# Kernel optimization log

Hardware: AMD Instinct MI355X
Metric: run time of the kernel (lower is better)

The kernel has to match this reference:

```python
import jax, jax.numpy as jnp
import numpy as np

B, D_MODEL, N, H = 4, 256, 2048, 4
HEAD_DIM = D_MODEL // H  # 64


def _rotate_half(x):
    # x: [..., d] with d even; pairs (x1, x2) -> (-x2, x1)
    x = x.reshape(x.shape[:-1] + (x.shape[-1] // 2, 2))
    x1, x2 = x[..., 0], x[..., 1]
    return jnp.stack((-x2, x1), axis=-1).reshape(x.shape[:-2] + (-1,))


def _apply_rope(freqs, t):
    # freqs: [2, n, d] (cos, sin); t: [b, h, n, d]
    return t * freqs[0] + _rotate_half(t) * freqs[1]


def setup_inputs() -> dict:
    key = jax.random.key(0)
    ks = jax.random.split(key, 12)
    s = 0.02
    inp = {
        "query": jax.random.normal(ks[0], (B, D_MODEL, N), jnp.float32),
        "key": jax.random.normal(ks[1], (B, D_MODEL, N), jnp.float32),
        "value": jax.random.normal(ks[2], (B, D_MODEL, N), jnp.float32),
        "encoding": jax.random.normal(ks[3], (2, N, HEAD_DIM), jnp.float32),
        "Wq": jax.random.normal(ks[4], (D_MODEL, D_MODEL), jnp.float32) * s,
        "bq": jnp.zeros((D_MODEL,), jnp.float32),
        "Wk": jax.random.normal(ks[5], (D_MODEL, D_MODEL), jnp.float32) * s,
        "bk": jnp.zeros((D_MODEL,), jnp.float32),
        "Wv": jax.random.normal(ks[6], (D_MODEL, D_MODEL), jnp.float32) * s,
        "bv": jnp.zeros((D_MODEL,), jnp.float32),
        "Wm": jax.random.normal(ks[7], (D_MODEL, D_MODEL), jnp.float32) * s,
        "bm": jnp.zeros((D_MODEL,), jnp.float32),
    }
    return inp


def _proj(W, b, x):
    # 1x1 Conv1d == channel matmul: x [b, c_in, n] -> [b, c_out, n]
    return jnp.einsum('oi,bin->bon', W, x) + b[None, :, None]


def reference(query, key, value, encoding, Wq, bq, Wk, bk, Wv, bv, Wm, bm):
    b = query.shape[0]
    # project and split channels into (head_dim, heads): [b, d, h, n]
    q = _proj(Wq, bq, query).reshape(b, HEAD_DIM, H, -1)
    k = _proj(Wk, bk, key).reshape(b, HEAD_DIM, H, -1)
    v = _proj(Wv, bv, value).reshape(b, HEAD_DIM, H, -1)
    # RoPE on [b, h, n, d] layout
    q = jnp.transpose(_apply_rope(encoding, jnp.transpose(q, (0, 2, 3, 1))), (0, 3, 1, 2))
    k = jnp.transpose(_apply_rope(encoding, jnp.transpose(k, (0, 2, 3, 1))), (0, 3, 1, 2))
    # attention: scores [b, h, n, m]
    scores = jnp.einsum('bdhn,bdhm->bhnm', q, k) / jnp.sqrt(jnp.float32(HEAD_DIM))
    prob = jax.nn.softmax(scores, axis=-1)
    x = jnp.einsum('bhnm,bdhm->bdhn', prob, v)
    x = x.reshape(b, HEAD_DIM * H, -1)
    return _proj(Wm, bm, x)
```

## Files before the change

kernel.cpp:

```cpp
#include <hip/hip_runtime.h>
#include <stdint.h>

#define NSEQ 2048

typedef __attribute__((ext_vector_type(4))) float f32x4;
typedef __attribute__((ext_vector_type(8))) short s16x8;
typedef _Float16 f16x8 __attribute__((ext_vector_type(8)));

#define OFF_XT  0u
#define OFF_XA  0u
#define OFF_PO  4194304u
#define OFF_W   12582912u
#define OFF_QR  13107200u
#define OFF_KR  17301504u
#define OFF_VT  21495808u
#define OFF_M   25690112u
#define OFF_L   25952256u

__device__ __forceinline__ short f2h(float f) {
  _Float16 h = (_Float16)f;
  return __builtin_bit_cast(short, h);
}
__device__ __forceinline__ float h2f(short s) {
  return (float)__builtin_bit_cast(_Float16, s);
}
__device__ __forceinline__ int swz64(int row, int slot) {
  return row * 64 + ((slot ^ ((row >> 1) & 3)) << 4);
}
__device__ __forceinline__ int swz128(int row, int slot) {
  return row * 128 + ((slot ^ (row & 7)) << 4);
}
#define MFMA(a, b, c) __builtin_amdgcn_mfma_f32_16x16x32_f16(a, b, c, 0, 0, 0)

__global__ void k_convw(const float* __restrict__ Wq, const float* __restrict__ Wk,
                        const float* __restrict__ Wv, const float* __restrict__ Wm,
                        char* __restrict__ ws) {
  int o = blockIdx.x, which = blockIdx.y, i = threadIdx.x;
  const float* src = which == 0 ? Wq : which == 1 ? Wk : which == 2 ? Wv : Wm;
  short* dst = (short*)(ws + OFF_W) + which * 65536;
  float val = (which < 3) ? src[o * 256 + i] : src[o * 256 + ((i & 63) << 2) + (i >> 6)];
  dst[o * 256 + i] = f2h(val);
}

__global__ __launch_bounds__(256) void k_trans(const float* __restrict__ q,
    const float* __restrict__ k, const float* __restrict__ v, char* __restrict__ ws) {
  int tensor = blockIdx.z >> 2, b = blockIdx.z & 3;
  const float* src = tensor == 0 ? q : (tensor == 1 ? k : v);
  short* dst = (short*)(ws + OFF_XT) + (tensor * 4 + b) * 524288;
  int n0 = blockIdx.x * 64, i0 = blockIdx.y * 64;
  __shared__ float tile[64][65];
  int t = threadIdx.x;
  int nl = t & 63, ib = (t >> 6) * 16;
#pragma unroll
  for (int r = 0; r < 16; ++r)
    tile[ib + r][nl] = src[(b * 256 + i0 + ib + r) * 2048 + n0 + nl];
  __syncthreads();
  int nr = t >> 2, ic = (t & 3) * 16;
  short tmp[16];
#pragma unroll
  for (int j = 0; j < 16; ++j) tmp[j] = f2h(tile[ic + j][nr]);
  short* dp = &dst[(n0 + nr) * 256 + i0 + ic];
  *(s16x8*)dp = *(const s16x8*)&tmp[0];
  *(s16x8*)(dp + 8) = *(const s16x8*)&tmp[8];
}

__device__ __forceinline__ void gemm128(const short* __restrict__ W, const short* __restrict__ X,
                                        int o0, int n0, short* As, short* Bs, f32x4 acc[4][4]) {
  int t = threadIdx.x;
  int lane = t & 63, g = lane >> 4, c = lane & 15, wave = t >> 6;
  int wo = (wave >> 1) * 64, wn = (wave & 1) * 64;
  int row = t >> 2, slot = t & 3;
  for (int kk = 0; kk < 8; ++kk) {
    __syncthreads();
    int koff = kk * 32 + slot * 8;
    *(s16x8*)((char*)As + swz64(row, slot))      = *(const s16x8*)&W[(o0 + row) * 256 + koff];
    *(s16x8*)((char*)As + swz64(row + 64, slot)) = *(const s16x8*)&W[(o0 + row + 64) * 256 + koff];
    *(s16x8*)((char*)Bs + swz64(row, slot))      = *(const s16x8*)&X[(n0 + row) * 256 + koff];
    *(s16x8*)((char*)Bs + swz64(row + 64, slot)) = *(const s16x8*)&X[(n0 + row + 64) * 256 + koff];
    __syncthreads();
    f16x8 af[4], bfr[4];
#pragma unroll
    for (int f = 0; f < 4; ++f) {
      af[f]  = *(const f16x8*)((char*)As + swz64(wo + f * 16 + c, g));
      bfr[f] = *(const f16x8*)((char*)Bs + swz64(wn + f * 16 + c, g));
    }
#pragma unroll
    for (int i = 0; i < 4; ++i)
#pragma unroll
      for (int j = 0; j < 4; ++j)
        acc[i][j] = MFMA(af[i], bfr[j], acc[i][j]);
  }
}

__global__ __launch_bounds__(256) void k_proj(const float* __restrict__ enc,
    const float* __restrict__ bq, const float* __restrict__ bk, const float* __restrict__ bv,
    char* __restrict__ ws) {
  int proj = blockIdx.z >> 2, b = blockIdx.z & 3;
  const short* W = (const short*)(ws + OFF_W) + proj * 65536;
  const short* X = (const short*)(ws + OFF_XT) + (proj * 4 + b) * 524288;
  int o0 = blockIdx.y * 128, n0 = blockIdx.x * 128;
  __shared__ short As[128 * 32], Bs[128 * 32];
  f32x4 acc[4][4] = {};
  gemm128(W, X, o0, n0, As, Bs, acc);
  int t = threadIdx.x, lane = t & 63, g = lane >> 4, c = lane & 15, wave = t >> 6;
  int wo = (wave >> 1) * 64, wn = (wave & 1) * 64;
  const float* bias = proj == 0 ? bq : (proj == 1 ? bk : bv);
  if (proj < 2) {
    short* dst = (short*)(ws + (proj == 0 ? OFF_QR : OFF_KR));
    float scale = proj == 0 ? 0.125f : 1.0f;
    float sgn = (g & 1) ? 1.0f : -1.0f;
#pragma unroll
    for (int i = 0; i < 4; ++i) {
      int ob = o0 + wo + i * 16 + g * 4;
      int d = ob >> 2;
#pragma unroll
      for (int j = 0; j < 4; ++j) {
        int n = n0 + wn + j * 16 + c;
        float cv = enc[n * 64 + d], sv = enc[131072 + n * 64 + d];
#pragma unroll
        for (int r = 0; r < 4; ++r) {
          float val = acc[i][j][r] + bias[ob + r];
          float par = __shfl_xor(val, 16, 64);
          float res = (val * cv + sgn * par * sv) * scale;
          dst[((b * 4 + r) * 2048 + n) * 64 + d] = f2h(res);
        }
      }
    }
  } else {
    short* dst = (short*)(ws + OFF_VT);
#pragma unroll
    for (int i = 0; i < 4; ++i) {
      int ob = o0 + wo + i * 16 + g * 4;
      int d = ob >> 2;
#pragma unroll
      for (int j = 0; j < 4; ++j) {
        int n = n0 + wn + j * 16 + c;
#pragma unroll
        for (int r = 0; r < 4; ++r) {
          float val = acc[i][j][r] + bias[ob + r];
          dst[((b * 4 + r) * 64 + d) * 2048 + n] = f2h(val);
        }
      }
    }
  }
}

__global__ __launch_bounds__(256, 4) void k_attn(char* __restrict__ ws) {
  int bh = blockIdx.y, ms = blockIdx.z;
  int t = threadIdx.x, wave = t >> 6, lane = t & 63, g = lane >> 4, c = lane & 15;
  int nw = blockIdx.x * 64 + wave * 16;
  const short* Q = (const short*)(ws + OFF_QR) + bh * 131072;
  const short* K = (const short*)(ws + OFF_KR) + bh * 131072;
  const short* V = (const short*)(ws + OFF_VT) + bh * 131072;
  __shared__ short Ks[64 * 64], Vs[64 * 64], Ps[4][16 * 64];
  char* Pb = (char*)Ps[wave];
  f16x8 qf0 = *(const f16x8*)&Q[(nw + c) * 64 + g * 8];
  f16x8 qf1 = *(const f16x8*)&Q[(nw + c) * 64 + 32 + g * 8];
  f32x4 po[4] = {};
  float mrun[4], lrun[4];
#pragma unroll
  for (int r = 0; r < 4; ++r) { mrun[r] = -1e30f; lrun[r] = 0.f; }
  int sr = t >> 3, sl = t & 7;
  const int mb = ms * 1024;

  s16x8 rk0, rk1, rv0, rv1, sk0, sk1, sv0, sv1;
  auto LD = [&](int m0, s16x8& a, s16x8& b2, s16x8& c2, s16x8& d2) {
    a  = *(const s16x8*)&K[(m0 + sr) * 64 + sl * 8];
    b2 = *(const s16x8*)&K[(m0 + sr + 32) * 64 + sl * 8];
    c2 = *(const s16x8*)&V[sr * 2048 + m0 + sl * 8];
    d2 = *(const s16x8*)&V[(sr + 32) * 2048 + m0 + sl * 8];
  };
  auto ST = [&](const s16x8& a, const s16x8& b2, const s16x8& c2, const s16x8& d2) {
    *(s16x8*)((char*)Ks + swz128(sr, sl))      = a;
    *(s16x8*)((char*)Ks + swz128(sr + 32, sl)) = b2;
    *(s16x8*)((char*)Vs + swz128(sr, sl))      = c2;
    *(s16x8*)((char*)Vs + swz128(sr + 32, sl)) = d2;
  };
  auto COMPUTE = [&]() {
    f32x4 s[4] = {};
    __builtin_amdgcn_s_setprio(1);
#pragma unroll
    for (int fj = 0; fj < 4; ++fj) {
      f16x8 k0 = *(const f16x8*)((char*)Ks + swz128(fj * 16 + c, g));
      f16x8 k1 = *(const f16x8*)((char*)Ks + swz128(fj * 16 + c, 4 + g));
      s[fj] = MFMA(qf0, k0, s[fj]);
      s[fj] = MFMA(qf1, k1, s[fj]);
    }
    __builtin_amdgcn_s_setprio(0);
    float pm[4], nm[4], corr[4], rs[4];
#pragma unroll
    for (int r = 0; r < 4; ++r) {
      pm[r] = fmaxf(fmaxf(s[0][r], s[1][r]), fmaxf(s[2][r], s[3][r]));
#pragma unroll
      for (int d_ = 1; d_ < 16; d_ <<= 1) pm[r] = fmaxf(pm[r], __shfl_xor(pm[r], d_, 64));
      nm[r] = fmaxf(mrun[r], pm[r]);
      corr[r] = __expf(mrun[r] - nm[r]);
      mrun[r] = nm[r];
      rs[r] = 0.f;
    }
    float p[4][4];
#pragma unroll
    for (int fj = 0; fj < 4; ++fj)
#pragma unroll
      for (int r = 0; r < 4; ++r) {
        p[fj][r] = __expf(s[fj][r] - nm[r]);
        rs[r] += p[fj][r];
      }
#pragma unroll
    for (int r = 0; r < 4; ++r) {
#pragma unroll
      for (int d_ = 1; d_ < 16; d_ <<= 1) rs[r] += __shfl_xor(rs[r], d_, 64);
      lrun[r] = lrun[r] * corr[r] + rs[r];
    }
#pragma unroll
    for (int fd = 0; fd < 4; ++fd)
#pragma unroll
      for (int r = 0; r < 4; ++r) po[fd][r] *= corr[r];
#pragma unroll
    for (int fj = 0; fj < 4; ++fj)
#pragma unroll
      for (int r = 0; r < 4; ++r) {
        int rr = g * 4 + r, mm = fj * 16 + c;
        *(short*)(Pb + swz128(rr, mm >> 3) + (mm & 7) * 2) = f2h(p[fj][r]);
      }
    asm volatile("s_waitcnt lgkmcnt(0)" ::: "memory");
    __builtin_amdgcn_sched_barrier(0);
    f16x8 pa0 = *(const f16x8*)(Pb + swz128(c, g));
    f16x8 pa1 = *(const f16x8*)(Pb + swz128(c, 4 + g));
    __builtin_amdgcn_s_setprio(1);
#pragma unroll
    for (int fd = 0; fd < 4; ++fd) {
      int dd = fd * 16 + c;
      f16x8 vb0 = *(const f16x8*)((char*)Vs + swz128(dd, g));
      f16x8 vb1 = *(const f16x8*)((char*)Vs + swz128(dd, 4 + g));
      po[fd] = MFMA(pa0, vb0, po[fd]);
      po[fd] = MFMA(pa1, vb1, po[fd]);
    }
    __builtin_amdgcn_s_setprio(0);
  };

  LD(mb, rk0, rk1, rv0, rv1);
  for (int tt = 0; tt < 16; tt += 2) {
    __syncthreads();
    ST(rk0, rk1, rv0, rv1);
    LD(mb + (tt + 1) * 64, sk0, sk1, sv0, sv1);
    __syncthreads();
    COMPUTE();
    __syncthreads();
    ST(sk0, sk1, sv0, sv1);
    if (tt + 2 < 16) LD(mb + (tt + 2) * 64, rk0, rk1, rv0, rv1);
    __syncthreads();
    COMPUTE();
  }

  short* PO = (short*)(ws + OFF_PO);
  float* Mm = (float*)(ws + OFF_M);
  float* Ll = (float*)(ws + OFF_L);
  int base = (ms * 16 + bh) * 2048;
#pragma unroll
  for (int fd = 0; fd < 4; ++fd) {
    int d = fd * 16 + c;
#pragma unroll
    for (int r = 0; r < 4; ++r) {
      int n = nw + g * 4 + r;
      PO[(base + n) * 64 + d] = f2h(po[fd][r] / lrun[r]);
    }
  }
  if (c == 0) {
#pragma unroll
    for (int r = 0; r < 4; ++r) {
      int n = nw + g * 4 + r;
      Mm[base + n] = mrun[r];
      Ll[base + n] = lrun[r];
    }
  }
}

__global__ __launch_bounds__(256) void k_comb(char* __restrict__ ws) {
  int t = threadIdx.x;
  int row = blockIdx.x * 32 + (t >> 3);
  int bh = row >> 11, n = row & 2047;
  int dc = (t & 7) * 8;
  const short* PO = (const short*)(ws + OFF_PO);
  const float* Mm = (const float*)(ws + OFF_M);
  const float* Ll = (const float*)(ws + OFF_L);
  float m1 = Mm[row], m2 = Mm[32768 + row];
  float l1 = Ll[row], l2 = Ll[32768 + row];
  float M = fmaxf(m1, m2);
  float w1 = l1 * __expf(m1 - M), w2 = l2 * __expf(m2 - M);
  float inv = 1.f / (w1 + w2);
  float a1 = w1 * inv, a2 = w2 * inv;
  s16x8 o1 = *(const s16x8*)&PO[row * 64 + dc];
  s16x8 o2 = *(const s16x8*)&PO[(32768 + row) * 64 + dc];
  short res[8];
#pragma unroll
  for (int j = 0; j < 8; ++j) res[j] = f2h(a1 * h2f(o1[j]) + a2 * h2f(o2[j]));
  short* XA = (short*)(ws + OFF_XA);
  int b = bh >> 2, h = bh & 3;
  *(s16x8*)&XA[(b * 2048 + n) * 256 + h * 64 + dc] = *(const s16x8*)res;
}

__global__ __launch_bounds__(256) void k_final(const float* __restrict__ bm,
    float* __restrict__ out, char* __restrict__ ws) {
  int b = blockIdx.z;
  const short* W = (const short*)(ws + OFF_W) + 3 * 65536;
  const short* X = (const short*)(ws + OFF_XA) + b * 524288;
  int o0 = blockIdx.y * 128, n0 = blockIdx.x * 128;
  __shared__ short As[128 * 32], Bs[128 * 32];
  f32x4 acc[4][4] = {};
  gemm128(W, X, o0, n0, As, Bs, acc);
  int t = threadIdx.x, lane = t & 63, g = lane >> 4, c = lane & 15, wave = t >> 6;
  int wo = (wave >> 1) * 64, wn = (wave & 1) * 64;
#pragma unroll
  for (int i = 0; i < 4; ++i) {
    int ob = o0 + wo + i * 16 + g * 4;
#pragma unroll
    for (int j = 0; j < 4; ++j) {
      int n = n0 + wn + j * 16 + c;
#pragma unroll
      for (int r = 0; r < 4; ++r)
        out[(b * 256 + ob + r) * 2048 + n] = acc[i][j][r] + bm[ob + r];
    }
  }
}

extern "C" void kernel_launch(void* const* d_in, const int* in_sizes, int n_in,
                              void* d_out, int out_size, void* d_ws, size_t ws_size,
                              hipStream_t stream) {
  (void)in_sizes; (void)n_in; (void)out_size; (void)ws_size;
  const float* q   = (const float*)d_in[0];
  const float* k   = (const float*)d_in[1];
  const float* v   = (const float*)d_in[2];
  const float* enc = (const float*)d_in[3];
  const float* Wq  = (const float*)d_in[4];
  const float* bq  = (const float*)d_in[5];
  const float* Wk  = (const float*)d_in[6];
  const float* bk  = (const float*)d_in[7];
  const float* Wv  = (const float*)d_in[8];
  const float* bv  = (const float*)d_in[9];
  const float* Wm  = (const float*)d_in[10];
  const float* bm  = (const float*)d_in[11];
  char* ws = (char*)d_ws;
  float* out = (float*)d_out;
  hipLaunchKernelGGL(k_convw, dim3(256, 4), dim3(256), 0, stream, Wq, Wk, Wv, Wm, ws);
  hipLaunchKernelGGL(k_trans, dim3(32, 4, 12), dim3(256), 0, stream, q, k, v, ws);
  hipLaunchKernelGGL(k_proj, dim3(16, 2, 12), dim3(256), 0, stream, enc, bq, bk, bv, ws);
  hipLaunchKernelGGL(k_attn, dim3(32, 16, 2), dim3(256), 0, stream, ws);
  hipLaunchKernelGGL(k_comb, dim3(1024), dim3(256), 0, stream, ws);
  hipLaunchKernelGGL(k_final, dim3(16, 2, 4), dim3(256), 0, stream, bm, out, ws);
}
```

Baseline: 182.5 us.

## Transpose score MFMA, use exp2 softmax with lazy rescale, widen GEMM K-tile

The attention kernel computes S^T so each lane owns one query row. Row max and sum then need only two cross-lane shuffles instead of four per row. The log2(e) factor is folded into the Q scale so softmax can use exp2f, and the running max is only rescaled when some row's new max exceeds the old one by a threshold, tested with a wave-wide vote. The projection GEMMs load 64-wide K tiles with swz128, halving the number of K iterations and barriers. The trade-offs are extra LDS use, per-row correction broadcasts through shuffles, and fp16 P values that can grow up to 2^11.5 before rescaling, which risks reduced precision.

New measurement: 161.5 us. -11.5%, faster.

```diff
diff --git a/kernel.cpp b/kernel.cpp
--- a/kernel.cpp
+++ b/kernel.cpp
@@ -24,9 +24,6 @@
 __device__ __forceinline__ float h2f(short s) {
   return (float)__builtin_bit_cast(_Float16, s);
 }
-__device__ __forceinline__ int swz64(int row, int slot) {
-  return row * 64 + ((slot ^ ((row >> 1) & 3)) << 4);
-}
 __device__ __forceinline__ int swz128(int row, int slot) {
   return row * 128 + ((slot ^ (row & 7)) << 4);
 }
@@ -69,26 +66,32 @@
   int t = threadIdx.x;
   int lane = t & 63, g = lane >> 4, c = lane & 15, wave = t >> 6;
   int wo = (wave >> 1) * 64, wn = (wave & 1) * 64;
-  int row = t >> 2, slot = t & 3;
-  for (int kk = 0; kk < 8; ++kk) {
-    __syncthreads();
-    int koff = kk * 32 + slot * 8;
-    *(s16x8*)((char*)As + swz64(row, slot))      = *(const s16x8*)&W[(o0 + row) * 256 + koff];
-    *(s16x8*)((char*)As + swz64(row + 64, slot)) = *(const s16x8*)&W[(o0 + row + 64) * 256 + koff];
-    *(s16x8*)((char*)Bs + swz64(row, slot))      = *(const s16x8*)&X[(n0 + row) * 256 + koff];
-    *(s16x8*)((char*)Bs + swz64(row + 64, slot)) = *(const s16x8*)&X[(n0 + row + 64) * 256 + koff];
-    __syncthreads();
-    f16x8 af[4], bfr[4];
-#pragma unroll
-    for (int f = 0; f < 4; ++f) {
-      af[f]  = *(const f16x8*)((char*)As + swz64(wo + f * 16 + c, g));
-      bfr[f] = *(const f16x8*)((char*)Bs + swz64(wn + f * 16 + c, g));
-    }
-#pragma unroll
-    for (int i = 0; i < 4; ++i)
-#pragma unroll
-      for (int j = 0; j < 4; ++j)
-        acc[i][j] = MFMA(af[i], bfr[j], acc[i][j]);
+  int row = t >> 1, half = t & 1;
+  for (int kk = 0; kk < 4; ++kk) {
+    __syncthreads();
+    int koff = kk * 64 + half * 32;
+    const short* wsrc = &W[(o0 + row) * 256 + koff];
+    const short* xsrc = &X[(n0 + row) * 256 + koff];
+#pragma unroll
+    for (int q4 = 0; q4 < 4; ++q4) {
+      *(s16x8*)((char*)As + swz128(row, half * 4 + q4)) = *(const s16x8*)(wsrc + q4 * 8);
+      *(s16x8*)((char*)Bs + swz128(row, half * 4 + q4)) = *(const s16x8*)(xsrc + q4 * 8);
+    }
+    __syncthreads();
+#pragma unroll
+    for (int ks = 0; ks < 2; ++ks) {
+      f16x8 af[4], bfr[4];
+#pragma unroll
+      for (int f = 0; f < 4; ++f) {
+        af[f]  = *(const f16x8*)((char*)As + swz128(wo + f * 16 + c, ks * 4 + g));
+        bfr[f] = *(const f16x8*)((char*)Bs + swz128(wn + f * 16 + c, ks * 4 + g));
+      }
+#pragma unroll
+      for (int i = 0; i < 4; ++i)
+#pragma unroll
+        for (int j = 0; j < 4; ++j)
+          acc[i][j] = MFMA(af[i], bfr[j], acc[i][j]);
+    }
   }
 }
 
@@ -99,15 +102,15 @@
   const short* W = (const short*)(ws + OFF_W) + proj * 65536;
   const short* X = (const short*)(ws + OFF_XT) + (proj * 4 + b) * 524288;
   int o0 = blockIdx.y * 128, n0 = blockIdx.x * 128;
-  __shared__ short As[128 * 32], Bs[128 * 32];
+  __shared__ short As[128 * 64], Bs[128 * 64];
   f32x4 acc[4][4] = {};
   gemm128(W, X, o0, n0, As, Bs, acc);
   int t = threadIdx.x, lane = t & 63, g = lane >> 4, c = lane & 15, wave = t >> 6;
   int wo = (wave >> 1) * 64, wn = (wave & 1) * 64;
   const float* bias = proj == 0 ? bq : (proj == 1 ? bk : bv);
   if (proj < 2) {
-    short* dst = (short*)(ws + (proj == 0 ? OFF_QR : OFF_KR));
-    float scale = proj == 0 ? 0.125f : 1.0f;
+    short* dst0 = (short*)(ws + (proj == 0 ? OFF_QR : OFF_KR));
+    float scale = proj == 0 ? 0.18033688f : 1.0f;
     float sgn = (g & 1) ? 1.0f : -1.0f;
 #pragma unroll
     for (int i = 0; i < 4; ++i) {
@@ -122,7 +125,7 @@
           float val = acc[i][j][r] + bias[ob + r];
           float par = __shfl_xor(val, 16, 64);
           float res = (val * cv + sgn * par * sv) * scale;
-          dst[((b * 4 + r) * 2048 + n) * 64 + d] = f2h(res);
+          dst0[((b * 4 + r) * 2048 + n) * 64 + d] = f2h(res);
         }
       }
     }
@@ -157,24 +160,23 @@
   f16x8 qf0 = *(const f16x8*)&Q[(nw + c) * 64 + g * 8];
   f16x8 qf1 = *(const f16x8*)&Q[(nw + c) * 64 + 32 + g * 8];
   f32x4 po[4] = {};
-  float mrun[4], lrun[4];
-#pragma unroll
-  for (int r = 0; r < 4; ++r) { mrun[r] = -1e30f; lrun[r] = 0.f; }
+  float mrun = -1e30f, lrun = 0.f;
   int sr = t >> 3, sl = t & 7;
   const int mb = ms * 1024;
-
-  s16x8 rk0, rk1, rv0, rv1, sk0, sk1, sv0, sv1;
-  auto LD = [&](int m0, s16x8& a, s16x8& b2, s16x8& c2, s16x8& d2) {
-    a  = *(const s16x8*)&K[(m0 + sr) * 64 + sl * 8];
-    b2 = *(const s16x8*)&K[(m0 + sr + 32) * 64 + sl * 8];
-    c2 = *(const s16x8*)&V[sr * 2048 + m0 + sl * 8];
-    d2 = *(const s16x8*)&V[(sr + 32) * 2048 + m0 + sl * 8];
+  int bsrc = g * 16 + g * 4;
+
+  s16x8 RA[4], RB[4];
+  auto LD = [&](int m0, s16x8* R) {
+    R[0] = *(const s16x8*)&K[(m0 + sr) * 64 + sl * 8];
+    R[1] = *(const s16x8*)&K[(m0 + sr + 32) * 64 + sl * 8];
+    R[2] = *(const s16x8*)&V[sr * 2048 + m0 + sl * 8];
+    R[3] = *(const s16x8*)&V[(sr + 32) * 2048 + m0 + sl * 8];
   };
-  auto ST = [&](const s16x8& a, const s16x8& b2, const s16x8& c2, const s16x8& d2) {
-    *(s16x8*)((char*)Ks + swz128(sr, sl))      = a;
-    *(s16x8*)((char*)Ks + swz128(sr + 32, sl)) = b2;
-    *(s16x8*)((char*)Vs + swz128(sr, sl))      = c2;
-    *(s16x8*)((char*)Vs + swz128(sr + 32, sl)) = d2;
+  auto ST = [&](const s16x8* R) {
+    *(s16x8*)((char*)Ks + swz128(sr, sl))      = R[0];
+    *(s16x8*)((char*)Ks + swz128(sr + 32, sl)) = R[1];
+    *(s16x8*)((char*)Vs + swz128(sr, sl))      = R[2];
+    *(s16x8*)((char*)Vs + swz128(sr + 32, sl)) = R[3];
   };
   auto COMPUTE = [&]() {
     f32x4 s[4] = {};
@@ -183,45 +185,49 @@
     for (int fj = 0; fj < 4; ++fj) {
       f16x8 k0 = *(const f16x8*)((char*)Ks + swz128(fj * 16 + c, g));
       f16x8 k1 = *(const f16x8*)((char*)Ks + swz128(fj * 16 + c, 4 + g));
-      s[fj] = MFMA(qf0, k0, s[fj]);
-      s[fj] = MFMA(qf1, k1, s[fj]);
+      s[fj] = MFMA(k0, qf0, s[fj]);
+      s[fj] = MFMA(k1, qf1, s[fj]);
     }
     __builtin_amdgcn_s_setprio(0);
-    float pm[4], nm[4], corr[4], rs[4];
-#pragma unroll
-    for (int r = 0; r < 4; ++r) {
-      pm[r] = fmaxf(fmaxf(s[0][r], s[1][r]), fmaxf(s[2][r], s[3][r]));
-#pragma unroll
-      for (int d_ = 1; d_ < 16; d_ <<= 1) pm[r] = fmaxf(pm[r], __shfl_xor(pm[r], d_, 64));
-      nm[r] = fmaxf(mrun[r], pm[r]);
-      corr[r] = __expf(mrun[r] - nm[r]);
-      mrun[r] = nm[r];
-      rs[r] = 0.f;
-    }
-    float p[4][4];
+    float t0 = fmaxf(fmaxf(s[0][0], s[0][1]), fmaxf(s[0][2], s[0][3]));
+    float t1 = fmaxf(fmaxf(s[1][0], s[1][1]), fmaxf(s[1][2], s[1][3]));
+    float t2 = fmaxf(fmaxf(s[2][0], s[2][1]), fmaxf(s[2][2], s[2][3]));
+    float t3 = fmaxf(fmaxf(s[3][0], s[3][1]), fmaxf(s[3][2], s[3][3]));
+    float rmax = fmaxf(fmaxf(t0, t1), fmaxf(t2, t3));
+    rmax = fmaxf(rmax, __shfl_xor(rmax, 16, 64));
+    rmax = fmaxf(rmax, __shfl_xor(rmax, 32, 64));
+    if (__any(rmax > mrun + 11.5f)) {
+      float nm = fmaxf(mrun, rmax);
+      float corr = exp2f(mrun - nm);
+      mrun = nm;
+      lrun *= corr;
+#pragma unroll
+      for (int r = 0; r < 4; ++r) {
+        float corr_r = __shfl(corr, bsrc + r, 64);
+#pragma unroll
+        for (int fd = 0; fd < 4; ++fd) po[fd][r] *= corr_r;
+      }
+    }
+    float p[4][4], rs = 0.f;
+#pragma unroll
+    for (int fj = 0; fj < 4; ++fj) {
+      f32x4 pv;
+#pragma unroll
+      for (int r = 0; r < 4; ++r) {
+        pv[r] = exp2f(s[fj][r] - mrun);
+        p[fj][r] = pv[r];
+      }
+      rs += (pv[0] + pv[1]) + (pv[2] + pv[3]);
+    }
+    rs += __shfl_xor(rs, 16, 64);
+    rs += __shfl_xor(rs, 32, 64);
+    lrun += rs;
 #pragma unroll
     for (int fj = 0; fj < 4; ++fj)
 #pragma unroll
       for (int r = 0; r < 4; ++r) {
-        p[fj][r] = __expf(s[fj][r] - nm[r]);
-        rs[r] += p[fj][r];
-      }
-#pragma unroll
-    for (int r = 0; r < 4; ++r) {
-#pragma unroll
-      for (int d_ = 1; d_ < 16; d_ <<= 1) rs[r] += __shfl_xor(rs[r], d_, 64);
-      lrun[r] = lrun[r] * corr[r] + rs[r];
-    }
-#pragma unroll
-    for (int fd = 0; fd < 4; ++fd)
-#pragma unroll
-      for (int r = 0; r < 4; ++r) po[fd][r] *= corr[r];
-#pragma unroll
-    for (int fj = 0; fj < 4; ++fj)
-#pragma unroll
-      for (int r = 0; r < 4; ++r) {
-        int rr = g * 4 + r, mm = fj * 16 + c;
-        *(short*)(Pb + swz128(rr, mm >> 3) + (mm & 7) * 2) = f2h(p[fj][r]);
+        int mm = fj * 16 + g * 4 + r;
+        *(short*)(Pb + swz128(c, mm >> 3) + (mm & 7) * 2) = f2h(p[fj][r]);
       }
     asm volatile("s_waitcnt lgkmcnt(0)" ::: "memory");
     __builtin_amdgcn_sched_barrier(0);
@@ -239,16 +245,16 @@
     __builtin_amdgcn_s_setprio(0);
   };
 
-  LD(mb, rk0, rk1, rv0, rv1);
+  LD(mb, RA);
   for (int tt = 0; tt < 16; tt += 2) {
     __syncthreads();
-    ST(rk0, rk1, rv0, rv1);
-    LD(mb + (tt + 1) * 64, sk0, sk1, sv0, sv1);
+    ST(RA);
+    LD(mb + (tt + 1) * 64, RB);
     __syncthreads();
     COMPUTE();
     __syncthreads();
-    ST(sk0, sk1, sv0, sv1);
-    if (tt + 2 < 16) LD(mb + (tt + 2) * 64, rk0, rk1, rv0, rv1);
+    ST(RB);
+    if (tt + 2 < 16) LD(mb + (tt + 2) * 64, RA);
     __syncthreads();
     COMPUTE();
   }
@@ -257,22 +263,21 @@
   float* Mm = (float*)(ws + OFF_M);
   float* Ll = (float*)(ws + OFF_L);
   int base = (ms * 16 + bh) * 2048;
+  float li[4];
+#pragma unroll
+  for (int r = 0; r < 4; ++r) li[r] = 1.0f / __shfl(lrun, bsrc + r, 64);
 #pragma unroll
   for (int fd = 0; fd < 4; ++fd) {
     int d = fd * 16 + c;
 #pragma unroll
     for (int r = 0; r < 4; ++r) {
       int n = nw + g * 4 + r;
-      PO[(base + n) * 64 + d] = f2h(po[fd][r] / lrun[r]);
-    }
-  }
-  if (c == 0) {
-#pragma unroll
-    for (int r = 0; r < 4; ++r) {
-      int n = nw + g * 4 + r;
-      Mm[base + n] = mrun[r];
-      Ll[base + n] = lrun[r];
-    }
+      PO[(base + n) * 64 + d] = f2h(po[fd][r] * li[r]);
+    }
+  }
+  if (g == 0) {
+    Mm[base + nw + c] = mrun;
+    Ll[base + nw + c] = lrun;
   }
 }
 
@@ -287,7 +292,7 @@
   float m1 = Mm[row], m2 = Mm[32768 + row];
   float l1 = Ll[row], l2 = Ll[32768 + row];
   float M = fmaxf(m1, m2);
-  float w1 = l1 * __expf(m1 - M), w2 = l2 * __expf(m2 - M);
+  float w1 = l1 * exp2f(m1 - M), w2 = l2 * exp2f(m2 - M);
   float inv = 1.f / (w1 + w2);
   float a1 = w1 * inv, a2 = w2 * inv;
   s16x8 o1 = *(const s16x8*)&PO[row * 64 + dc];
@@ -306,7 +311,7 @@
   const short* W = (const short*)(ws + OFF_W) + 3 * 65536;
   const short* X = (const short*)(ws + OFF_XA) + b * 524288;
   int o0 = blockIdx.y * 128, n0 = blockIdx.x * 128;
-  __shared__ short As[128 * 32], Bs[128 * 32];
+  __shared__ short As[128 * 64], Bs[128 * 64];
   f32x4 acc[4][4] = {};
   gemm128(W, X, o0, n0, As, Bs, acc);
   int t = threadIdx.x, lane = t & 63, g = lane >> 4, c = lane & 15, wave = t >> 6;
```
